# Kernel optimization log

Hardware: AMD Instinct MI355X
Metric: run time of the kernel (lower is better)

The kernel has to match this reference:

```python
import jax, jax.numpy as jnp
import numpy as np

ALPHA = 0.1
MARGIN = 1.0
SLOPE = 0.2  # LeakyReLU negative_slope
OFFSET = 1.0e6

def leaky(x):
    return jnp.where(x >= 0, x, SLOPE * x)

def _xavier(key, shape, gain=np.sqrt(2.0)):
    fan_out, fan_in = shape[0], shape[1]
    std = gain * np.sqrt(2.0 / (fan_in + fan_out))
    return jax.random.normal(key, shape, dtype=jnp.float32) * std

def setup_inputs() -> dict:
    key = jax.random.key(0)
    ks = jax.random.split(key, 8)
    B, F, T, D, H = 32768, 128, 32, 16, 10
    return {
        "X": jax.random.normal(ks[0], (B, F), dtype=jnp.float32),
        "affine_weights": jax.random.normal(ks[1], (T, F, D), dtype=jnp.float32),
        "W0": _xavier(ks[2], (H, D)),
        "W1": _xavier(ks[3], (H, H)),
        "W2": _xavier(ks[4], (H, H)),
        "W3": _xavier(ks[5], (H, H)),
        "Wh": _xavier(ks[6], (T, H)),
        "bh": jnp.zeros((T,), dtype=jnp.float32),
    }

def reference(X, affine_weights, W0, W1, W2, W3, Wh, bh):
    T = affine_weights.shape[0]
    # goad_transforms: x_trans [B, trans_dim, n_trans]; labels[b,t] = t (implicit)
    x_trans = jnp.einsum('bn,ant->bta', X, affine_weights)
    # ConvNet encoder, kernel_size=1 convs == per-position channel matmuls
    h = jnp.einsum('od,bdt->bot', W0, x_trans)
    for W in (W1, W2, W3):
        h = jnp.einsum('od,bdt->bot', W, leaky(h))
    rep = h                                   # [B, H, T]
    # head: LeakyReLU + Conv1d(H->T, bias=True)
    pred = jnp.einsum('oh,bht->bot', Wh, leaky(rep)) + bh[None, :, None]  # [B, T, T]
    batch_rep = jnp.transpose(rep, (0, 2, 1))  # [B, T, H]
    # CrossEntropy(reduction='none') with labels[b,t]=t -> -diag of log_softmax over class dim
    logp = jax.nn.log_softmax(pred, axis=1)
    loss_ce = -jnp.diagonal(logp, axis1=1, axis2=2)          # [B, T]
    # triplet center loss
    means = jnp.mean(batch_rep, axis=0)                       # [T, H]
    res = jnp.sum((batch_rep[:, :, None, :] - means[None, None, :, :]) ** 2, axis=-1)  # [B,T,T]
    pos = jnp.diagonal(res, axis1=1, axis2=2)                 # [B, T]
    neg = jnp.min(res + jnp.eye(T, dtype=res.dtype) * OFFSET, axis=-1)  # [B, T]
    loss_tc = jnp.mean(jnp.maximum(pos + MARGIN - neg, 0.0))  # scalar
    loss = jnp.mean(ALPHA * loss_tc + loss_ce, axis=1)        # [B]
    return batch_rep, loss
```

## Files before the change

kernel.cpp:

```cpp
#include <hip/hip_runtime.h>

typedef __attribute__((ext_vector_type(8))) short bf16x8;
typedef __attribute__((ext_vector_type(4))) float f32x4;

#define BTOT 32768
#define FDIM 128
#define TDIM 32
#define DDIM 16
#define HDIM 10
#define CDIM 320
#define ALPHA_C 0.1f
#define MARGIN_C 1.0f
#define SLOPE_C 0.2f
#define OFFSET_C 1.0e6f

#define WS_A0P  0
#define WS_MEAN 32768
#define WS_TC   33088
#define WS_CE   33152

__device__ __forceinline__ float leaky(float x) { return fmaxf(x, SLOPE_C * x); }

__device__ __forceinline__ unsigned short f2bf(float f) {
    unsigned int u = __float_as_uint(f);
    u += 0x7fffu + ((u >> 16) & 1u);
    return (unsigned short)(u >> 16);
}

__device__ __forceinline__ f32x4 mfma32(bf16x8 a, bf16x8 b, f32x4 c) {
    return __builtin_amdgcn_mfma_f32_16x16x32_bf16(a, b, c, 0, 0, 0);
}

__device__ __forceinline__ void leaky_pack(f32x4 v, unsigned& p0, unsigned& p1) {
    float a0 = leaky(v[0]), a1 = leaky(v[1]), a2 = leaky(v[2]), a3 = leaky(v[3]);
    asm("v_cvt_pk_bf16_f32 %0, %1, %2" : "=v"(p0) : "v"(a0), "v"(a1));
    asm("v_cvt_pk_bf16_f32 %0, %1, %2" : "=v"(p1) : "v"(a2), "v"(a3));
}

__device__ __forceinline__ bf16x8 build_bfrag(unsigned p0, unsigned p1, int g, int r16) {
    int s0 = ((2 * g) * 16 + r16) & 63;
    int s1 = ((2 * g + 1) * 16 + r16) & 63;
    unsigned w0 = (unsigned)__shfl((int)p0, s0, 64);
    unsigned w1 = (unsigned)__shfl((int)p1, s0, 64);
    unsigned w2 = (unsigned)__shfl((int)p0, s1, 64);
    unsigned w3 = (unsigned)__shfl((int)p1, s1, 64);
    unsigned zm = (g < 2) ? 0xFFFFFFFFu : 0u;
    union { unsigned u[4]; bf16x8 v; } r;
    r.u[0] = w0 & zm; r.u[1] = w1 & zm; r.u[2] = w2 & zm; r.u[3] = w3 & zm;
    return r.v;
}

__global__ void prep_kernel(const float* __restrict__ aw, const float* __restrict__ W0,
                            unsigned short* __restrict__ a0p) {
    int idx = blockIdx.x * blockDim.x + threadIdx.x;
    if (idx >= 65536) return;
    int n = idx & 127, o = (idx >> 7) & 15, t = idx >> 11;
    unsigned short r = 0;
    if (o < 10) {
        const float* a = aw + ((size_t)t * FDIM + n) * DDIM;
        const float* w = W0 + o * DDIM;
        float s = 0.f;
#pragma unroll
        for (int d = 0; d < DDIM; ++d) s += a[d] * w[d];
        r = f2bf(s);
    }
    a0p[idx] = r;
}

__global__ __launch_bounds__(256, 4) void gemm0_fused(
    const float* __restrict__ X, const unsigned short* __restrict__ a0p,
    const float* __restrict__ W1, const float* __restrict__ W2,
    const float* __restrict__ W3, const float* __restrict__ Wh,
    const float* __restrict__ bh,
    float* __restrict__ rep, float* __restrict__ ce_acc,
    float* __restrict__ mean_acc)
{
    __shared__ unsigned short xs[32][136];
    __shared__ unsigned short w1x[16][32], w2x[16][32], w3x[16][32], whx[32][32];
    __shared__ float mred[2][16][12];

    int tid = threadIdx.x;
    int b0 = (blockIdx.x >> 1) * 32;
    int thalf = blockIdx.x & 1;

#pragma unroll
    for (int k = 0; k < 4; ++k) {
        int idx = tid + k * 256;
        int row = idx >> 5, col4 = idx & 31;
        float4 v = reinterpret_cast<const float4*>(X + (size_t)(b0 + row) * FDIM)[col4];
        unsigned p0, p1;
        asm("v_cvt_pk_bf16_f32 %0, %1, %2" : "=v"(p0) : "v"(v.x), "v"(v.y));
        asm("v_cvt_pk_bf16_f32 %0, %1, %2" : "=v"(p1) : "v"(v.z), "v"(v.w));
        uint2 pk; pk.x = p0; pk.y = p1;
        *reinterpret_cast<uint2*>(&xs[row][col4 * 4]) = pk;
    }
#pragma unroll
    for (int k = 0; k < 2; ++k) {
        int i = tid + k * 256;
        int o = i >> 5, kk = i & 31;
        bool in10 = (o < 10 && kk < 10);
        w1x[o][kk] = in10 ? f2bf(W1[o * 10 + kk]) : (unsigned short)0;
        w2x[o][kk] = in10 ? f2bf(W2[o * 10 + kk]) : (unsigned short)0;
        w3x[o][kk] = in10 ? f2bf(W3[o * 10 + kk]) : (unsigned short)0;
    }
#pragma unroll
    for (int k = 0; k < 4; ++k) {
        int i = tid + k * 256;
        int o = i >> 5, kk = i & 31;
        whx[o][kk] = (kk < 10) ? f2bf(Wh[o * 10 + kk]) : (unsigned short)0;
    }
    __syncthreads();

    int lane = tid & 63, w = __builtin_amdgcn_readfirstlane(tid >> 6);
    int r16 = lane & 15, g = lane >> 4;
    int bsub = w >> 1, tq = w & 1;
    int bglob = b0 + bsub * 16 + r16;

    bf16x8 xf[4];
#pragma unroll
    for (int s = 0; s < 4; ++s)
        xf[s] = *reinterpret_cast<const bf16x8*>(&xs[bsub * 16 + r16][s * 32 + g * 8]);

    bf16x8 w1f = *reinterpret_cast<const bf16x8*>(&w1x[r16][g * 8]);
    bf16x8 w2f = *reinterpret_cast<const bf16x8*>(&w2x[r16][g * 8]);
    bf16x8 w3f = *reinterpret_cast<const bf16x8*>(&w3x[r16][g * 8]);
    bf16x8 whAf = *reinterpret_cast<const bf16x8*>(&whx[r16][g * 8]);
    bf16x8 whBf = *reinterpret_cast<const bf16x8*>(&whx[16 + r16][g * 8]);
    f32x4 bhA, bhB;
#pragma unroll
    for (int r = 0; r < 4; ++r) { bhA[r] = bh[g * 4 + r]; bhB[r] = bh[16 + g * 4 + r]; }
    const f32x4 zero4 = {0.f, 0.f, 0.f, 0.f};

    float ce_local = 0.f;

    for (int tt2 = 0; tt2 < 2; ++tt2) {
#pragma unroll
        for (int q = 0; q < 4; ++q) {
            int tloc = tq * 8 + tt2 * 4 + q;
            int t = thalf * 16 + tloc;
            const bf16x8* ap = reinterpret_cast<const bf16x8*>(
                a0p + ((size_t)t * 16 + r16) * 128);
            f32x4 accA = zero4, accB = zero4;
            accA = mfma32(ap[0 * 4 + g], xf[0], accA);
            accB = mfma32(ap[1 * 4 + g], xf[1], accB);
            accA = mfma32(ap[2 * 4 + g], xf[2], accA);
            accB = mfma32(ap[3 * 4 + g], xf[3], accB);
            f32x4 acc;
#pragma unroll
            for (int r = 0; r < 4; ++r) acc[r] = accA[r] + accB[r];

            unsigned p0, p1;
            leaky_pack(acc, p0, p1);
            bf16x8 bf = build_bfrag(p0, p1, g, r16);
            f32x4 d1 = mfma32(w1f, bf, zero4);
            leaky_pack(d1, p0, p1);
            bf = build_bfrag(p0, p1, g, r16);
            f32x4 d2 = mfma32(w2f, bf, zero4);
            leaky_pack(d2, p0, p1);
            bf = build_bfrag(p0, p1, g, r16);
            f32x4 d3 = mfma32(w3f, bf, zero4);

            float* rp = rep + (size_t)bglob * CDIM + t * HDIM + g * 4;
            if (g < 2) {
                float2 v0; v0.x = d3[0]; v0.y = d3[1];
                float2 v1; v1.x = d3[2]; v1.y = d3[3];
                reinterpret_cast<float2*>(rp)[0] = v0;
                reinterpret_cast<float2*>(rp)[1] = v1;
            } else if (g == 2) {
                float2 v0; v0.x = d3[0]; v0.y = d3[1];
                reinterpret_cast<float2*>(rp)[0] = v0;
            }

            float m0 = d3[0], m1 = d3[1], m2 = d3[2], m3 = d3[3];
#pragma unroll
            for (int msk = 1; msk < 16; msk <<= 1) {
                m0 += __shfl_xor(m0, msk, 64);
                m1 += __shfl_xor(m1, msk, 64);
                m2 += __shfl_xor(m2, msk, 64);
                m3 += __shfl_xor(m3, msk, 64);
            }
            if (r16 == 0 && g < 3) {
                float4 mv; mv.x = m0; mv.y = m1; mv.z = m2; mv.w = m3;
                *reinterpret_cast<float4*>(&mred[bsub][tloc][g * 4]) = mv;
            }

            leaky_pack(d3, p0, p1);
            bf = build_bfrag(p0, p1, g, r16);
            f32x4 pA = mfma32(whAf, bf, bhA);
            f32x4 pB = mfma32(whBf, bf, bhB);

            float mx = fmaxf(fmaxf(fmaxf(pA[0], pA[1]), fmaxf(pA[2], pA[3])),
                             fmaxf(fmaxf(pB[0], pB[1]), fmaxf(pB[2], pB[3])));
            mx = fmaxf(mx, __shfl_xor(mx, 16, 64));
            mx = fmaxf(mx, __shfl_xor(mx, 32, 64));
            float se = __expf(pA[0] - mx) + __expf(pA[1] - mx) +
                       __expf(pA[2] - mx) + __expf(pA[3] - mx) +
                       __expf(pB[0] - mx) + __expf(pB[1] - mx) +
                       __expf(pB[2] - mx) + __expf(pB[3] - mx);
            se += __shfl_xor(se, 16, 64);
            se += __shfl_xor(se, 32, 64);
            float lse = mx + __logf(se);
            float pr = thalf ? pB[q] : pA[q];
            float ptv = __shfl(pr, (tq * 2 + tt2) * 16 + r16, 64);
            ce_local += lse - ptv;
        }
    }

    if (g == 0) atomicAdd(&ce_acc[bglob], ce_local);
    __syncthreads();
    for (int i = tid; i < 16 * HDIM; i += 256) {
        int tloc = i / 10, o = i - tloc * 10;
        atomicAdd(&mean_acc[(thalf * 16 + tloc) * HDIM + o],
                  mred[0][tloc][o] + mred[1][tloc][o]);
    }
}

__global__ __launch_bounds__(256) void tc_kernel(const float* __restrict__ rep,
    const float* __restrict__ mean_acc, float* __restrict__ tc_sum)
{
    __shared__ float tile[32][CDIM];
    __shared__ float mm[CDIM];
    __shared__ float msq[TDIM];
    __shared__ float wpart[4];
    int tid = threadIdx.x;
    int b0 = blockIdx.x * 32;

    for (int i = tid; i < CDIM; i += 256) mm[i] = mean_acc[i] * (1.f / BTOT);
    const float4* src = reinterpret_cast<const float4*>(rep + (size_t)b0 * CDIM);
#pragma unroll
    for (int k = 0; k < 10; ++k) {
        int idx = tid + k * 256;
        int row = idx / 80, col4 = idx - row * 80;
        *reinterpret_cast<float4*>(&tile[row][col4 * 4]) = src[idx];
    }
    __syncthreads();
    if (tid < TDIM) {
        float s = 0.f;
#pragma unroll
        for (int h = 0; h < HDIM; ++h) { float v = mm[tid * HDIM + h]; s += v * v; }
        msq[tid] = s;
    }
    __syncthreads();

    int t = tid & 31, bg = tid >> 5;
    float rv[4][HDIM], rsq[4];
#pragma unroll
    for (int j = 0; j < 4; ++j) {
        const float* rp = &tile[bg * 4 + j][t * HDIM];
        float s = 0.f;
#pragma unroll
        for (int q = 0; q < 5; ++q) {
            float2 v = reinterpret_cast<const float2*>(rp)[q];
            rv[j][2 * q] = v.x; rv[j][2 * q + 1] = v.y;
            s += v.x * v.x + v.y * v.y;
        }
        rsq[j] = s;
    }
    float pos[4], neg[4];
#pragma unroll
    for (int j = 0; j < 4; ++j) { pos[j] = 0.f; neg[j] = 1e30f; }
#pragma unroll 4
    for (int c = 0; c < TDIM; ++c) {
        float m0[HDIM];
#pragma unroll
        for (int q = 0; q < 5; ++q) {
            float2 v = reinterpret_cast<const float2*>(&mm[c * HDIM])[q];
            m0[2 * q] = v.x; m0[2 * q + 1] = v.y;
        }
        float mq = msq[c];
        bool isT = (c == t);
#pragma unroll
        for (int j = 0; j < 4; ++j) {
            float dot = 0.f;
#pragma unroll
            for (int h = 0; h < HDIM; ++h) dot += rv[j][h] * m0[h];
            float s = rsq[j] - 2.f * dot + mq;
            if (isT) pos[j] = s;
            float s2 = isT ? s + OFFSET_C : s;
            neg[j] = fminf(neg[j], s2);
        }
    }
    float hs = 0.f;
#pragma unroll
    for (int j = 0; j < 4; ++j) hs += fmaxf(pos[j] + MARGIN_C - neg[j], 0.f);
#pragma unroll
    for (int m = 1; m < 64; m <<= 1) hs += __shfl_xor(hs, m, 64);
    int lane = tid & 63, w = tid >> 6;
    if (lane == 0) wpart[w] = hs;
    __syncthreads();
    if (tid == 0) atomicAdd(tc_sum, wpart[0] + wpart[1] + wpart[2] + wpart[3]);
}

__global__ void final_kernel(const float* __restrict__ ce_acc,
                             const float* __restrict__ tc_sum, float* __restrict__ loss)
{
    int b = blockIdx.x * blockDim.x + threadIdx.x;
    if (b < BTOT)
        loss[b] = ALPHA_C * (tc_sum[0] * (1.f / ((float)BTOT * TDIM)))
                + ce_acc[b] * (1.f / TDIM);
}

extern "C" void kernel_launch(void* const* d_in, const int* in_sizes, int n_in,
                              void* d_out, int out_size, void* d_ws, size_t ws_size,
                              hipStream_t stream) {
    const float* X  = (const float*)d_in[0];
    const float* aw = (const float*)d_in[1];
    const float* W0 = (const float*)d_in[2];
    const float* W1 = (const float*)d_in[3];
    const float* W2 = (const float*)d_in[4];
    const float* W3 = (const float*)d_in[5];
    const float* Wh = (const float*)d_in[6];
    const float* bh = (const float*)d_in[7];
    float* ws = (float*)d_ws;
    unsigned short* a0p = (unsigned short*)(ws + WS_A0P);
    float* mean_acc = ws + WS_MEAN;
    float* tc_sum   = ws + WS_TC;
    float* ce_acc   = ws + WS_CE;
    float* out_rep = (float*)d_out;
    float* loss = out_rep + (size_t)BTOT * TDIM * HDIM;

    hipMemsetAsync(mean_acc, 0, (384 + BTOT) * sizeof(float), stream);
    prep_kernel<<<256, 256, 0, stream>>>(aw, W0, a0p);
    gemm0_fused<<<2048, 256, 0, stream>>>(X, a0p, W1, W2, W3, Wh, bh,
                                          out_rep, ce_acc, mean_acc);
    tc_kernel<<<BTOT / 32, 256, 0, stream>>>(out_rep, mean_acc, tc_sum);
    final_kernel<<<BTOT / 256, 256, 0, stream>>>(ce_acc, tc_sum, loss);
}
```

Before: 99.73 us.

## Interleave two transform chains per iteration and move mean reduction to separate kernel

The fused kernel now processes two transforms at a time, interleaving their MFMA chains and shuffles so independent work can hide the latency of the serial dependency chain. The per-block column-mean reduction (shuffle tree, shared memory, syncthreads, atomics) is removed from the main kernel. It is replaced by a separate meanred_kernel that rereads rep from global memory. The trade-off is an extra launch and an extra full read of rep, about 42 MB, in exchange for a lighter main kernel with more instruction-level parallelism.

```diff
diff --git a/kernel.cpp b/kernel.cpp
--- a/kernel.cpp
+++ b/kernel.cpp
@@ -50,6 +50,10 @@
     return r.v;
 }
 
+__device__ __forceinline__ float pick4(f32x4 v, int r) {
+    return (r & 2) ? ((r & 1) ? v[3] : v[2]) : ((r & 1) ? v[1] : v[0]);
+}
+
 __global__ void prep_kernel(const float* __restrict__ aw, const float* __restrict__ W0,
                             unsigned short* __restrict__ a0p) {
     int idx = blockIdx.x * blockDim.x + threadIdx.x;
@@ -72,12 +76,10 @@
     const float* __restrict__ W1, const float* __restrict__ W2,
     const float* __restrict__ W3, const float* __restrict__ Wh,
     const float* __restrict__ bh,
-    float* __restrict__ rep, float* __restrict__ ce_acc,
-    float* __restrict__ mean_acc)
+    float* __restrict__ rep, float* __restrict__ ce_acc)
 {
     __shared__ unsigned short xs[32][136];
     __shared__ unsigned short w1x[16][32], w2x[16][32], w3x[16][32], whx[32][32];
-    __shared__ float mred[2][16][12];
 
     int tid = threadIdx.x;
     int b0 = (blockIdx.x >> 1) * 32;
@@ -133,86 +135,120 @@
 
     float ce_local = 0.f;
 
-    for (int tt2 = 0; tt2 < 2; ++tt2) {
-#pragma unroll
-        for (int q = 0; q < 4; ++q) {
-            int tloc = tq * 8 + tt2 * 4 + q;
-            int t = thalf * 16 + tloc;
-            const bf16x8* ap = reinterpret_cast<const bf16x8*>(
-                a0p + ((size_t)t * 16 + r16) * 128);
-            f32x4 accA = zero4, accB = zero4;
-            accA = mfma32(ap[0 * 4 + g], xf[0], accA);
-            accB = mfma32(ap[1 * 4 + g], xf[1], accB);
-            accA = mfma32(ap[2 * 4 + g], xf[2], accA);
-            accB = mfma32(ap[3 * 4 + g], xf[3], accB);
-            f32x4 acc;
-#pragma unroll
-            for (int r = 0; r < 4; ++r) acc[r] = accA[r] + accB[r];
-
-            unsigned p0, p1;
-            leaky_pack(acc, p0, p1);
-            bf16x8 bf = build_bfrag(p0, p1, g, r16);
-            f32x4 d1 = mfma32(w1f, bf, zero4);
-            leaky_pack(d1, p0, p1);
-            bf = build_bfrag(p0, p1, g, r16);
-            f32x4 d2 = mfma32(w2f, bf, zero4);
-            leaky_pack(d2, p0, p1);
-            bf = build_bfrag(p0, p1, g, r16);
-            f32x4 d3 = mfma32(w3f, bf, zero4);
-
-            float* rp = rep + (size_t)bglob * CDIM + t * HDIM + g * 4;
-            if (g < 2) {
-                float2 v0; v0.x = d3[0]; v0.y = d3[1];
-                float2 v1; v1.x = d3[2]; v1.y = d3[3];
-                reinterpret_cast<float2*>(rp)[0] = v0;
-                reinterpret_cast<float2*>(rp)[1] = v1;
-            } else if (g == 2) {
-                float2 v0; v0.x = d3[0]; v0.y = d3[1];
-                reinterpret_cast<float2*>(rp)[0] = v0;
-            }
-
-            float m0 = d3[0], m1 = d3[1], m2 = d3[2], m3 = d3[3];
-#pragma unroll
-            for (int msk = 1; msk < 16; msk <<= 1) {
-                m0 += __shfl_xor(m0, msk, 64);
-                m1 += __shfl_xor(m1, msk, 64);
-                m2 += __shfl_xor(m2, msk, 64);
-                m3 += __shfl_xor(m3, msk, 64);
-            }
-            if (r16 == 0 && g < 3) {
-                float4 mv; mv.x = m0; mv.y = m1; mv.z = m2; mv.w = m3;
-                *reinterpret_cast<float4*>(&mred[bsub][tloc][g * 4]) = mv;
-            }
-
-            leaky_pack(d3, p0, p1);
-            bf = build_bfrag(p0, p1, g, r16);
-            f32x4 pA = mfma32(whAf, bf, bhA);
-            f32x4 pB = mfma32(whBf, bf, bhB);
-
-            float mx = fmaxf(fmaxf(fmaxf(pA[0], pA[1]), fmaxf(pA[2], pA[3])),
-                             fmaxf(fmaxf(pB[0], pB[1]), fmaxf(pB[2], pB[3])));
-            mx = fmaxf(mx, __shfl_xor(mx, 16, 64));
-            mx = fmaxf(mx, __shfl_xor(mx, 32, 64));
-            float se = __expf(pA[0] - mx) + __expf(pA[1] - mx) +
-                       __expf(pA[2] - mx) + __expf(pA[3] - mx) +
-                       __expf(pB[0] - mx) + __expf(pB[1] - mx) +
-                       __expf(pB[2] - mx) + __expf(pB[3] - mx);
-            se += __shfl_xor(se, 16, 64);
-            se += __shfl_xor(se, 32, 64);
-            float lse = mx + __logf(se);
-            float pr = thalf ? pB[q] : pA[q];
-            float ptv = __shfl(pr, (tq * 2 + tt2) * 16 + r16, 64);
-            ce_local += lse - ptv;
+    for (int u = 0; u < 4; ++u) {
+        int ttA = 2 * u, ttB = 2 * u + 1;
+        int tA = thalf * 16 + tq * 8 + ttA;
+        int tB = tA + 1;
+        const bf16x8* apA = reinterpret_cast<const bf16x8*>(a0p + ((size_t)tA * 16 + r16) * 128);
+        const bf16x8* apB = reinterpret_cast<const bf16x8*>(a0p + ((size_t)tB * 16 + r16) * 128);
+
+        f32x4 aA0 = zero4, aA1 = zero4, aB0 = zero4, aB1 = zero4;
+        aA0 = mfma32(apA[0 * 4 + g], xf[0], aA0);
+        aB0 = mfma32(apB[0 * 4 + g], xf[0], aB0);
+        aA1 = mfma32(apA[1 * 4 + g], xf[1], aA1);
+        aB1 = mfma32(apB[1 * 4 + g], xf[1], aB1);
+        aA0 = mfma32(apA[2 * 4 + g], xf[2], aA0);
+        aB0 = mfma32(apB[2 * 4 + g], xf[2], aB0);
+        aA1 = mfma32(apA[3 * 4 + g], xf[3], aA1);
+        aB1 = mfma32(apB[3 * 4 + g], xf[3], aB1);
+        f32x4 accA, accB;
+#pragma unroll
+        for (int r = 0; r < 4; ++r) { accA[r] = aA0[r] + aA1[r]; accB[r] = aB0[r] + aB1[r]; }
+
+        unsigned pa0, pa1, pb0, pb1;
+        leaky_pack(accA, pa0, pa1);
+        leaky_pack(accB, pb0, pb1);
+        bf16x8 bfA = build_bfrag(pa0, pa1, g, r16);
+        bf16x8 bfB = build_bfrag(pb0, pb1, g, r16);
+        f32x4 d1A = mfma32(w1f, bfA, zero4);
+        f32x4 d1B = mfma32(w1f, bfB, zero4);
+        leaky_pack(d1A, pa0, pa1);
+        leaky_pack(d1B, pb0, pb1);
+        bfA = build_bfrag(pa0, pa1, g, r16);
+        bfB = build_bfrag(pb0, pb1, g, r16);
+        f32x4 d2A = mfma32(w2f, bfA, zero4);
+        f32x4 d2B = mfma32(w2f, bfB, zero4);
+        leaky_pack(d2A, pa0, pa1);
+        leaky_pack(d2B, pb0, pb1);
+        bfA = build_bfrag(pa0, pa1, g, r16);
+        bfB = build_bfrag(pb0, pb1, g, r16);
+        f32x4 d3A = mfma32(w3f, bfA, zero4);
+        f32x4 d3B = mfma32(w3f, bfB, zero4);
+
+        float* rpA = rep + (size_t)bglob * CDIM + tA * HDIM + g * 4;
+        float* rpB = rep + (size_t)bglob * CDIM + tB * HDIM + g * 4;
+        if (g < 2) {
+            float2 v0, v1;
+            v0.x = d3A[0]; v0.y = d3A[1]; v1.x = d3A[2]; v1.y = d3A[3];
+            reinterpret_cast<float2*>(rpA)[0] = v0;
+            reinterpret_cast<float2*>(rpA)[1] = v1;
+            v0.x = d3B[0]; v0.y = d3B[1]; v1.x = d3B[2]; v1.y = d3B[3];
+            reinterpret_cast<float2*>(rpB)[0] = v0;
+            reinterpret_cast<float2*>(rpB)[1] = v1;
+        } else if (g == 2) {
+            float2 v0;
+            v0.x = d3A[0]; v0.y = d3A[1];
+            reinterpret_cast<float2*>(rpA)[0] = v0;
+            v0.x = d3B[0]; v0.y = d3B[1];
+            reinterpret_cast<float2*>(rpB)[0] = v0;
         }
+
+        leaky_pack(d3A, pa0, pa1);
+        leaky_pack(d3B, pb0, pb1);
+        bfA = build_bfrag(pa0, pa1, g, r16);
+        bfB = build_bfrag(pb0, pb1, g, r16);
+        f32x4 hA1 = mfma32(whAf, bfA, bhA);
+        f32x4 hB1 = mfma32(whAf, bfB, bhA);
+        f32x4 hA2 = mfma32(whBf, bfA, bhB);
+        f32x4 hB2 = mfma32(whBf, bfB, bhB);
+
+        float mxA = fmaxf(fmaxf(fmaxf(hA1[0], hA1[1]), fmaxf(hA1[2], hA1[3])),
+                          fmaxf(fmaxf(hA2[0], hA2[1]), fmaxf(hA2[2], hA2[3])));
+        float mxB = fmaxf(fmaxf(fmaxf(hB1[0], hB1[1]), fmaxf(hB1[2], hB1[3])),
+                          fmaxf(fmaxf(hB2[0], hB2[1]), fmaxf(hB2[2], hB2[3])));
+        mxA = fmaxf(mxA, __shfl_xor(mxA, 16, 64));
+        mxB = fmaxf(mxB, __shfl_xor(mxB, 16, 64));
+        mxA = fmaxf(mxA, __shfl_xor(mxA, 32, 64));
+        mxB = fmaxf(mxB, __shfl_xor(mxB, 32, 64));
+        float seA = __expf(hA1[0] - mxA) + __expf(hA1[1] - mxA) +
+                    __expf(hA1[2] - mxA) + __expf(hA1[3] - mxA) +
+                    __expf(hA2[0] - mxA) + __expf(hA2[1] - mxA) +
+                    __expf(hA2[2] - mxA) + __expf(hA2[3] - mxA);
+        float seB = __expf(hB1[0] - mxB) + __expf(hB1[1] - mxB) +
+                    __expf(hB1[2] - mxB) + __expf(hB1[3] - mxB) +
+                    __expf(hB2[0] - mxB) + __expf(hB2[1] - mxB) +
+                    __expf(hB2[2] - mxB) + __expf(hB2[3] - mxB);
+        seA += __shfl_xor(seA, 16, 64);
+        seB += __shfl_xor(seB, 16, 64);
+        seA += __shfl_xor(seA, 32, 64);
+        seB += __shfl_xor(seB, 32, 64);
+        float lseA = mxA + __logf(seA);
+        float lseB = mxB + __logf(seB);
+
+        int gsrc = tq * 2 + (u >> 1);
+        int regA = (u & 1) * 2;
+        float prA = pick4(thalf ? hA2 : hA1, regA);
+        float prB = pick4(thalf ? hB2 : hB1, regA + 1);
+        float ptA = __shfl(prA, gsrc * 16 + r16, 64);
+        float ptB = __shfl(prB, gsrc * 16 + r16, 64);
+        ce_local += (lseA - ptA) + (lseB - ptB);
     }
 
     if (g == 0) atomicAdd(&ce_acc[bglob], ce_local);
-    __syncthreads();
-    for (int i = tid; i < 16 * HDIM; i += 256) {
-        int tloc = i / 10, o = i - tloc * 10;
-        atomicAdd(&mean_acc[(thalf * 16 + tloc) * HDIM + o],
-                  mred[0][tloc][o] + mred[1][tloc][o]);
-    }
+}
+
+__global__ void meanred_kernel(const float* __restrict__ rep, float* __restrict__ mean_acc)
+{
+    int j = threadIdx.x;
+    const float* base = rep + (size_t)blockIdx.x * 128 * CDIM;
+    float s0 = 0, s1 = 0, s2 = 0, s3 = 0;
+    for (int b = 0; b < 128; b += 4) {
+        s0 += base[(size_t)(b + 0) * CDIM + j];
+        s1 += base[(size_t)(b + 1) * CDIM + j];
+        s2 += base[(size_t)(b + 2) * CDIM + j];
+        s3 += base[(size_t)(b + 3) * CDIM + j];
+    }
+    atomicAdd(&mean_acc[j], s0 + s1 + s2 + s3);
 }
 
 __global__ __launch_bounds__(256) void tc_kernel(const float* __restrict__ rep,
@@ -322,7 +358,8 @@
     hipMemsetAsync(mean_acc, 0, (384 + BTOT) * sizeof(float), stream);
     prep_kernel<<<256, 256, 0, stream>>>(aw, W0, a0p);
     gemm0_fused<<<2048, 256, 0, stream>>>(X, a0p, W1, W2, W3, Wh, bh,
-                                          out_rep, ce_acc, mean_acc);
+                                          out_rep, ce_acc);
+    meanred_kernel<<<256, 320, 0, stream>>>(out_rep, mean_acc);
     tc_kernel<<<BTOT / 32, 256, 0, stream>>>(out_rep, mean_acc, tc_sum);
     final_kernel<<<BTOT / 256, 256, 0, stream>>>(ce_acc, tc_sum, loss);
 }
```

New measurement: 100.3 us. Within noise of the previous version (+0.5%).
